# Optimization experiments

Hardware: AMD Instinct MI355X
Metric: run time of the kernel (lower is better)

Reference implementation:

```python
import jax, jax.numpy as jnp
import numpy as np

B_SZ, SEQ, H = 8, 1024, 2048
LN_EPS = 1e-6
CLIP = 1.0e6


def setup_inputs() -> dict:
    key = jax.random.key(0)
    ks = jax.random.split(key, 8)
    lecun = 1.0 / np.sqrt(H)
    return {
        "x": jax.random.normal(ks[0], (B_SZ, SEQ, H), dtype=jnp.float32),
        "context": jnp.zeros((B_SZ, H), dtype=jnp.float32),
        # learned params
        "A": -jax.random.uniform(ks[1], (H,), dtype=jnp.float32),  # diagonal decay (zeros-init in src; small negative for stable decay)
        "Bm": jax.random.normal(ks[2], (H, H), dtype=jnp.float32) * lecun,
        "Cm": jax.random.normal(ks[3], (H, H), dtype=jnp.float32) * lecun,
        "dt_kernel": jax.random.normal(ks[4], (H, 1), dtype=jnp.float32) * 0.02,
        "dt_bias": jnp.zeros((1,), dtype=jnp.float32),
        "gate_kernel": jax.random.normal(ks[5], (H, H), dtype=jnp.float32) * lecun,
        "gate_bias": jnp.zeros((H,), dtype=jnp.float32),
        "ln_scale": jnp.ones((H,), dtype=jnp.float32),
        "ln_bias": jnp.zeros((H,), dtype=jnp.float32),
    }


def _layernorm(x, scale, bias):
    mu = jnp.mean(x, axis=-1, keepdims=True)
    var = jnp.mean(jnp.square(x - mu), axis=-1, keepdims=True)
    return (x - mu) * jax.lax.rsqrt(var + LN_EPS) * scale + bias


def reference(x, context, A, Bm, Cm, dt_kernel, dt_bias, gate_kernel, gate_bias, ln_scale, ln_bias):
    xn = jnp.clip(_layernorm(x, ln_scale, ln_bias), -CLIP, CLIP)  # [B,S,H]
    xt = jnp.swapaxes(xn, 0, 1)  # time-major [S,B,H]

    def step(state, x_t):
        # x_t: [B,H]; delta: [B,1] from Dense(1)
        delta = jnp.exp(x_t @ dt_kernel + dt_bias)
        decay = jnp.exp(delta * A)                  # [B,H] via broadcast
        new_state = state * decay + x_t @ Bm        # [B,H]
        out = new_state @ Cm                        # [B,H]
        return new_state, out

    final_state, ys = jax.lax.scan(step, context, xt)
    outputs = jnp.swapaxes(ys, 0, 1)  # [B,S,H]
    gate = outputs @ gate_kernel + gate_bias
    outputs = outputs * jax.nn.sigmoid(gate)  # GLU
    # dropout deterministic (training=False) -> identity
    return outputs, final_state
```

## Files before the change

### kernel.cpp

```cpp
#include <hip/hip_runtime.h>
#include <hip/hip_bf16.h>

#define H_DIM 2048
#define B_SZ  8
#define SEQ   1024
#define M_DIM (B_SZ*SEQ)
#define KDIM  2048
#define NKT   (KDIM/64)
#define CCH   32
#define CLEN  (SEQ/CCH)

using f32x4 = __attribute__((ext_vector_type(4))) float;
using s16x8 = __attribute__((ext_vector_type(8))) short;

__device__ __forceinline__ float bf2f(unsigned short u) {
  unsigned int x = ((unsigned int)u) << 16;
  return __builtin_bit_cast(float, x);
}
__device__ __forceinline__ unsigned short f2bf(float f) {
  unsigned int x = __builtin_bit_cast(unsigned int, f);
  unsigned int r = (x + 0x7fffu + ((x >> 16) & 1u)) >> 16;
  return (unsigned short)r;
}

__device__ __forceinline__ void gl_lds16(const void* g, void* l) {
  __builtin_amdgcn_global_load_lds(
      (__attribute__((address_space(1))) void*)g,
      (__attribute__((address_space(3))) void*)l, 16, 0, 0);
}

__global__ __launch_bounds__(256) void transpose_kernel(
    const float* __restrict__ src, unsigned short* __restrict__ dst, int R, int C)
{
  __shared__ float t[32][33];
  int tx = threadIdx.x & 31, ty = threadIdx.x >> 5;
  int c0 = blockIdx.x << 5, r0 = blockIdx.y << 5;
#pragma unroll
  for (int i = 0; i < 32; i += 8)
    t[ty + i][tx] = src[(size_t)(r0 + ty + i) * C + (c0 + tx)];
  __syncthreads();
#pragma unroll
  for (int i = 0; i < 32; i += 8)
    dst[(size_t)(c0 + ty + i) * R + (r0 + tx)] = f2bf(t[tx][ty + i]);
}

__global__ __launch_bounds__(256) void ln_delta_kernel(
    const float* __restrict__ x, const float* __restrict__ lns,
    const float* __restrict__ lnb, const float* __restrict__ dtk,
    const float* __restrict__ dtb, unsigned short* __restrict__ xn,
    float* __restrict__ delta)
{
  const int row = blockIdx.x;
  const int tid = threadIdx.x;
  const float* xr = x + (size_t)row * H_DIM;
  float v[8];
  *(float4*)&v[0] = ((const float4*)xr)[tid * 2];
  *(float4*)&v[4] = ((const float4*)xr)[tid * 2 + 1];
  float s1 = 0.f, s2 = 0.f;
#pragma unroll
  for (int j = 0; j < 8; ++j) { s1 += v[j]; s2 += v[j] * v[j]; }
  __shared__ float red[8];
#pragma unroll
  for (int off = 32; off; off >>= 1) {
    s1 += __shfl_down(s1, off);
    s2 += __shfl_down(s2, off);
  }
  if ((tid & 63) == 0) { red[tid >> 6] = s1; red[4 + (tid >> 6)] = s2; }
  __syncthreads();
  float mean = (red[0] + red[1] + red[2] + red[3]) * (1.0f / H_DIM);
  float var  = (red[4] + red[5] + red[6] + red[7]) * (1.0f / H_DIM) - mean * mean;
  float rstd = rsqrtf(var + 1e-6f);

  float sc[8], bi[8], dk[8];
  *(float4*)&sc[0] = ((const float4*)lns)[tid * 2];
  *(float4*)&sc[4] = ((const float4*)lns)[tid * 2 + 1];
  *(float4*)&bi[0] = ((const float4*)lnb)[tid * 2];
  *(float4*)&bi[4] = ((const float4*)lnb)[tid * 2 + 1];
  *(float4*)&dk[0] = ((const float4*)dtk)[tid * 2];
  *(float4*)&dk[4] = ((const float4*)dtk)[tid * 2 + 1];

  float dot = 0.f;
  s16x8 o;
#pragma unroll
  for (int j = 0; j < 8; ++j) {
    float xv = (v[j] - mean) * rstd * sc[j] + bi[j];
    xv = fminf(fmaxf(xv, -1.0e6f), 1.0e6f);
    dot += xv * dk[j];
    o[j] = (short)f2bf(xv);
  }
  *(s16x8*)(xn + (size_t)row * H_DIM + tid * 8) = o;

  __syncthreads();
#pragma unroll
  for (int off = 32; off; off >>= 1) dot += __shfl_down(dot, off);
  if ((tid & 63) == 0) red[tid >> 6] = dot;
  __syncthreads();
  if (tid == 0)
    delta[row] = __expf(red[0] + red[1] + red[2] + red[3] + dtb[0]);
}

__global__ __launch_bounds__(256) void scan1_kernel(
    const unsigned short* __restrict__ U, const float* __restrict__ delta,
    const float* __restrict__ Adiag, float* __restrict__ Q, float* __restrict__ P)
{
  const int h = blockIdx.x * 1024 + threadIdx.x * 4;
  const int c = blockIdx.y, b = blockIdx.z;
  const float4 a = *(const float4*)(Adiag + h);
  const unsigned short* u = U + ((size_t)b * SEQ + c * CLEN) * H_DIM + h;
  const float* dl = delta + b * SEQ + c * CLEN;
  float4 st = {0.f, 0.f, 0.f, 0.f};
  float4 pr = {1.f, 1.f, 1.f, 1.f};
#pragma unroll 8
  for (int s = 0; s < CLEN; ++s) {
    const float d = dl[s];
    const ushort4 uv = *(const ushort4*)(u + (size_t)s * H_DIM);
    const float dx = __expf(d * a.x), dy = __expf(d * a.y);
    const float dz = __expf(d * a.z), dw = __expf(d * a.w);
    st.x = fmaf(st.x, dx, bf2f(uv.x)); st.y = fmaf(st.y, dy, bf2f(uv.y));
    st.z = fmaf(st.z, dz, bf2f(uv.z)); st.w = fmaf(st.w, dw, bf2f(uv.w));
    pr.x *= dx; pr.y *= dy; pr.z *= dz; pr.w *= dw;
  }
  const size_t idx = ((size_t)b * CCH + c) * H_DIM + h;
  *(float4*)(Q + idx) = st;
  *(float4*)(P + idx) = pr;
}

__global__ __launch_bounds__(256) void scan2_kernel(
    const float* __restrict__ Q, const float* __restrict__ P,
    const float* __restrict__ ctx, float* __restrict__ sIn,
    float* __restrict__ finalSt)
{
  const int h = blockIdx.x * 256 + threadIdx.x;
  const int b = blockIdx.y;
  float s = ctx[b * H_DIM + h];
#pragma unroll
  for (int c = 0; c < CCH; ++c) {
    const size_t idx = ((size_t)b * CCH + c) * H_DIM + h;
    sIn[idx] = s;
    s = fmaf(s, P[idx], Q[idx]);
  }
  finalSt[b * H_DIM + h] = s;
}

__global__ __launch_bounds__(256) void scan3_kernel(
    const unsigned short* __restrict__ U, const float* __restrict__ delta,
    const float* __restrict__ Adiag, const float* __restrict__ sIn,
    unsigned short* __restrict__ states)
{
  const int h = blockIdx.x * 1024 + threadIdx.x * 4;
  const int c = blockIdx.y, b = blockIdx.z;
  const float4 a = *(const float4*)(Adiag + h);
  const unsigned short* u = U + ((size_t)b * SEQ + c * CLEN) * H_DIM + h;
  unsigned short* so = states + ((size_t)b * SEQ + c * CLEN) * H_DIM + h;
  const float* dl = delta + b * SEQ + c * CLEN;
  float4 st = *(const float4*)(sIn + ((size_t)b * CCH + c) * H_DIM + h);
#pragma unroll 8
  for (int s = 0; s < CLEN; ++s) {
    const float d = dl[s];
    const ushort4 uv = *(const ushort4*)(u + (size_t)s * H_DIM);
    const float dx = __expf(d * a.x), dy = __expf(d * a.y);
    const float dz = __expf(d * a.z), dw = __expf(d * a.w);
    st.x = fmaf(st.x, dx, bf2f(uv.x)); st.y = fmaf(st.y, dy, bf2f(uv.y));
    st.z = fmaf(st.z, dz, bf2f(uv.z)); st.w = fmaf(st.w, dw, bf2f(uv.w));
    ushort4 ov = { f2bf(st.x), f2bf(st.y), f2bf(st.z), f2bf(st.w) };
    *(ushort4*)(so + (size_t)s * H_DIM) = ov;
  }
}


#define BARR()  __builtin_amdgcn_s_barrier();
#define LGKM0() asm volatile("s_waitcnt lgkmcnt(0)");
#define VMC(N)  asm volatile("s_waitcnt vmcnt(" #N ")" ::: "memory");

#define RD_A03(PA0, PA1) { _Pragma("unroll") for (int i_ = 0; i_ < 4; ++i_) { \
    a0[i_] = *(const s16x8*)((PA0) + i_ * 4096); \
    a1[i_] = *(const s16x8*)((PA1) + i_ * 4096); } }
#define RD_A47(PA0, PA1) { _Pragma("unroll") for (int i_ = 0; i_ < 4; ++i_) { \
    a0[i_] = *(const s16x8*)((PA0) + 16384 + i_ * 4096); \
    a1[i_] = *(const s16x8*)((PA1) + 16384 + i_ * 4096); } }
#define RD_B01(PB0, PB1) { _Pragma("unroll") for (int j_ = 0; j_ < 2; ++j_) { \
    bq0[j_] = *(const s16x8*)((PB0) + j_ * 8192); \
    bq1[j_] = *(const s16x8*)((PB1) + j_ * 8192); } }
#define RD_B23(PB0, PB1) { _Pragma("unroll") for (int j_ = 2; j_ < 4; ++j_) { \
    bq0[j_] = *(const s16x8*)((PB0) + j_ * 8192); \
    bq1[j_] = *(const s16x8*)((PB1) + j_ * 8192); } }

#define Q_MM(IB, JB) { __builtin_amdgcn_s_setprio(1); \
  _Pragma("unroll") for (int i_ = 0; i_ < 4; ++i_) \
  _Pragma("unroll") for (int j_ = 0; j_ < 2; ++j_) { \
    acc[(IB)+i_][(JB)+j_] = __builtin_amdgcn_mfma_f32_16x16x32_bf16(a0[i_], bq0[(JB)+j_], acc[(IB)+i_][(JB)+j_], 0, 0, 0); \
    acc[(IB)+i_][(JB)+j_] = __builtin_amdgcn_mfma_f32_16x16x32_bf16(a1[i_], bq1[(JB)+j_], acc[(IB)+i_][(JB)+j_], 0, 0, 0); } \
  __builtin_amdgcn_s_setprio(0); }

#define PH(QM) { BARR(); LGKM0(); QM; BARR(); }

#define STAGE_A(BUF, HH, TT) { const char* s_ = srcA + (HH) * 524288 + (TT) * 128; \
  char* d_ = ldsA + (BUF) * 32768 + (HH) * 16384 + tid16; \
  gl_lds16(s_, d_); gl_lds16(s_ + 262144, d_ + 8192); }
#define STAGE_B(BUF, HH, TT) { const char* s_ = srcB + (HH) * 524288 + (TT) * 128; \
  char* d_ = ldsB + (BUF) * 32768 + (HH) * 16384 + tid16; \
  gl_lds16(s_, d_); gl_lds16(s_ + 262144, d_ + 8192); }

template <int EPI>
__global__ __launch_bounds__(512, 2) void gemm8p(
    const char* __restrict__ Ab, const char* __restrict__ Bb,
    float* __restrict__ outF, unsigned short* __restrict__ outH,
    const unsigned short* __restrict__ Ybf, const float* __restrict__ gbias)
{
  extern __shared__ char lds[];
  char* ldsA = lds;
  char* ldsB = lds + 65536;

  const int tid  = threadIdx.x;
  const int lane = tid & 63, wid = tid >> 6;
  const int wr = wid >> 2, wc = wid & 3;
  const int fr = lane & 15, kq = lane >> 4;

  const int bid = blockIdx.x;
  const int xcd = bid & 7;
  const int li  = bid >> 3;
  const int bm  = (xcd >> 1) * 8 + (li & 7);
  const int bn  = (xcd & 1) * 4 + (li >> 3);

  const int grow = tid >> 3;
  const int gswz = ((tid & 7) ^ (grow & 7)) << 4;
  const char* srcA = Ab + ((size_t)(bm * 256 + grow)) * 4096 + gswz;
  const char* srcB = Bb + ((size_t)(bn * 256 + grow)) * 4096 + gswz;
  const int tid16 = tid << 4;

  const int sw0 = ((kq ^ (fr & 7)) << 4);
  const int sw1 = (((4 | kq) ^ (fr & 7)) << 4);
  const char* pa0b0 = ldsA + wr * 2048 + fr * 128 + sw0;
  const char* pa1b0 = ldsA + wr * 2048 + fr * 128 + sw1;
  const char* pa0b1 = pa0b0 + 32768;
  const char* pa1b1 = pa1b0 + 32768;
  const char* pb0b0 = ldsB + wc * 2048 + fr * 128 + sw0;
  const char* pb1b0 = ldsB + wc * 2048 + fr * 128 + sw1;
  const char* pb0b1 = pb0b0 + 32768;
  const char* pb1b1 = pb1b0 + 32768;

  f32x4 acc[8][4] = {};
  s16x8 a0[4], a1[4], bq0[4], bq1[4];

  STAGE_A(0, 0, 0); STAGE_B(0, 0, 0); STAGE_B(0, 1, 0); STAGE_A(0, 1, 0);
  STAGE_A(1, 0, 1); STAGE_B(1, 0, 1); STAGE_B(1, 1, 1);
  VMC(6);
  BARR();

  for (int t = 0; t < NKT / 2 - 1; ++t) {
    const int T0 = 2 * t;
    RD_A03(pa0b0, pa1b0); RD_B01(pb0b0, pb1b0);
    STAGE_A(1, 1, T0 + 1);
    PH(Q_MM(0, 0));
    RD_B23(pb0b0, pb1b0);
    STAGE_A(0, 0, T0 + 2);
    PH(Q_MM(0, 2));
    RD_A47(pa0b0, pa1b0);
    STAGE_B(0, 0, T0 + 2);
    PH(Q_MM(4, 0));
    STAGE_B(0, 1, T0 + 2);
    BARR(); Q_MM(4, 2); VMC(6); BARR();
    RD_A03(pa0b1, pa1b1); RD_B01(pb0b1, pb1b1);
    STAGE_A(0, 1, T0 + 2);
    PH(Q_MM(0, 0));
    RD_B23(pb0b1, pb1b1);
    STAGE_A(1, 0, T0 + 3);
    PH(Q_MM(0, 2));
    RD_A47(pa0b1, pa1b1);
    STAGE_B(1, 0, T0 + 3);
    PH(Q_MM(4, 0));
    STAGE_B(1, 1, T0 + 3);
    BARR(); Q_MM(4, 2); VMC(6); BARR();
  }

  RD_A03(pa0b0, pa1b0); RD_B01(pb0b0, pb1b0);
  STAGE_A(1, 1, 31);
  PH(Q_MM(0, 0));
  RD_B23(pb0b0, pb1b0);
  PH(Q_MM(0, 2));
  RD_A47(pa0b0, pa1b0);
  PH(Q_MM(4, 0));
  BARR(); Q_MM(4, 2); VMC(0); BARR();
  RD_A03(pa0b1, pa1b1); RD_B01(pb0b1, pb1b1);
  PH(Q_MM(0, 0));
  RD_B23(pb0b1, pb1b1);
  PH(Q_MM(0, 2));
  RD_A47(pa0b1, pa1b1);
  PH(Q_MM(4, 0));
  LGKM0();
  Q_MM(4, 2);

  __syncthreads();
  const int cr = (lane >> 4) << 2;
  const int cc = lane & 15;
  if constexpr (EPI == 1) {
#pragma unroll
    for (int i = 0; i < 8; ++i)
#pragma unroll
      for (int j = 0; j < 4; ++j)
#pragma unroll
        for (int r = 0; r < 4; ++r) {
          const int row = (2 * i + wr) * 16 + cr + r;
          const int col = (4 * j + wc) * 16 + cc;
          const int off = (row * 512 + col * 2) ^ ((row & 7) << 4);
          *(unsigned short*)(lds + off) = f2bf(acc[i][j][r]);
        }
    __syncthreads();
#pragma unroll
    for (int it = 0; it < 16; ++it) {
      const int L = it * 8192 + tid * 16;
      const int row = L >> 9, inrow = L & 511;
      const s16x8 v = *(const s16x8*)(lds + (L ^ ((row & 7) << 4)));
      *(s16x8*)(outH + ((size_t)(bm * 256 + row)) * H_DIM + bn * 256 + (inrow >> 1)) = v;
    }
  } else {
#pragma unroll
    for (int p = 0; p < 2; ++p) {
      if (p) __syncthreads();
#pragma unroll
      for (int i = 4 * p; i < 4 * p + 4; ++i)
#pragma unroll
        for (int j = 0; j < 4; ++j)
#pragma unroll
          for (int r = 0; r < 4; ++r) {
            const int lrow = (2 * i + wr) * 16 + cr + r - 128 * p;
            const int col = (4 * j + wc) * 16 + cc;
            const int off = (lrow * 1024 + col * 4) ^ ((lrow & 7) << 4);
            *(float*)(lds + off) = acc[i][j][r];
          }
      __syncthreads();
#pragma unroll
      for (int it = 0; it < 16; ++it) {
        const int L = it * 8192 + tid * 16;
        const int lrow = L >> 10, inrow = L & 1023;
        const f32x4 v = *(const f32x4*)(lds + (L ^ ((lrow & 7) << 4)));
        const size_t growg = (size_t)(bm * 256 + 128 * p + lrow);
        const int gcol = bn * 256 + (inrow >> 2);
        const float4 gb4 = *(const float4*)(gbias + gcol);
        const ushort4 y4 = *(const ushort4*)(Ybf + growg * H_DIM + gcol);
        float4 o;
        o.x = bf2f(y4.x) / (1.f + __expf(-(v[0] + gb4.x)));
        o.y = bf2f(y4.y) / (1.f + __expf(-(v[1] + gb4.y)));
        o.z = bf2f(y4.z) / (1.f + __expf(-(v[2] + gb4.z)));
        o.w = bf2f(y4.w) / (1.f + __expf(-(v[3] + gb4.w)));
        *(float4*)(outF + growg * H_DIM + gcol) = o;
      }
    }
  }
}

extern "C" void kernel_launch(void* const* d_in, const int* in_sizes, int n_in,
                              void* d_out, int out_size, void* d_ws, size_t ws_size,
                              hipStream_t stream) {
  (void)in_sizes; (void)n_in; (void)out_size; (void)ws_size;
  const float* x     = (const float*)d_in[0];
  const float* ctx   = (const float*)d_in[1];
  const float* Adiag = (const float*)d_in[2];
  const float* Bm    = (const float*)d_in[3];
  const float* Cm    = (const float*)d_in[4];
  const float* dtk   = (const float*)d_in[5];
  const float* dtb   = (const float*)d_in[6];
  const float* gk    = (const float*)d_in[7];
  const float* gb    = (const float*)d_in[8];
  const float* lns   = (const float*)d_in[9];
  const float* lnb   = (const float*)d_in[10];
  float* outF = (float*)d_out;

  char* ws = (char*)d_ws;
  unsigned short* xnY    = (unsigned short*)ws; ws += (size_t)M_DIM * H_DIM * 2;
  unsigned short* U      = (unsigned short*)ws; ws += (size_t)M_DIM * H_DIM * 2;
  unsigned short* states = (unsigned short*)ws; ws += (size_t)M_DIM * H_DIM * 2;
  unsigned short* T1     = (unsigned short*)ws; ws += (size_t)H_DIM * H_DIM * 2;
  unsigned short* T2     = (unsigned short*)ws; ws += (size_t)H_DIM * H_DIM * 2;
  unsigned short* T3     = (unsigned short*)ws; ws += (size_t)H_DIM * H_DIM * 2;
  float* delta           = (float*)ws;          ws += (size_t)M_DIM * 4;
  float* Qbuf            = (float*)ws;          ws += (size_t)B_SZ * CCH * H_DIM * 4;
  float* Pbuf            = (float*)ws;          ws += (size_t)B_SZ * CCH * H_DIM * 4;
  float* sInBuf          = (float*)ws;          ws += (size_t)B_SZ * CCH * H_DIM * 4;

  hipFuncSetAttribute((const void*)&gemm8p<1>,
                      hipFuncAttributeMaxDynamicSharedMemorySize, 131072);
  hipFuncSetAttribute((const void*)&gemm8p<2>,
                      hipFuncAttributeMaxDynamicSharedMemorySize, 131072);

  dim3 tb(256);
  transpose_kernel<<<dim3(64, 64), tb, 0, stream>>>(Bm, T1, H_DIM, H_DIM);
  transpose_kernel<<<dim3(64, 64), tb, 0, stream>>>(Cm, T2, H_DIM, H_DIM);
  transpose_kernel<<<dim3(64, 64), tb, 0, stream>>>(gk, T3, H_DIM, H_DIM);
  ln_delta_kernel<<<M_DIM, tb, 0, stream>>>(x, lns, lnb, dtk, dtb, xnY, delta);
  gemm8p<1><<<256, 512, 131072, stream>>>(
      (const char*)xnY, (const char*)T1, nullptr, U, nullptr, nullptr);
  scan1_kernel<<<dim3(H_DIM / 1024, CCH, B_SZ), tb, 0, stream>>>(
      U, delta, Adiag, Qbuf, Pbuf);
  scan2_kernel<<<dim3(H_DIM / 256, B_SZ), tb, 0, stream>>>(
      Qbuf, Pbuf, ctx, sInBuf, outF + (size_t)M_DIM * H_DIM);
  scan3_kernel<<<dim3(H_DIM / 1024, CCH, B_SZ), tb, 0, stream>>>(
      U, delta, Adiag, sInBuf, states);
  gemm8p<1><<<256, 512, 131072, stream>>>(
      (const char*)states, (const char*)T2, nullptr, xnY, nullptr, nullptr);
  gemm8p<2><<<256, 512, 131072, stream>>>(
      (const char*)xnY, (const char*)T3, outF, nullptr, xnY, gb);
}
```

Measured before the change: 257.3 us.

## Software-pipeline LDS fragment reads one phase ahead of MFMA in GEMM loop

Restructures the GEMM main loop so LDS fragment reads for the next MFMA phase are issued before the current phase's MFMAs, using separate register sets for the A and B fragments. The explicit lgkmcnt waits and the double barriers per phase are removed, leaving one vmcnt wait plus barrier per phase. The goal is to hide LDS read latency behind matrix math. In exchange it uses more fragment registers, which can raise register pressure at 2 waves per SIMD. LDS buffer reuse must stay correct under the looser barrier placement.

```diff
diff --git a/kernel.cpp b/kernel.cpp
--- a/kernel.cpp
+++ b/kernel.cpp
@@ -169,30 +169,21 @@
 
 
 #define BARR()  __builtin_amdgcn_s_barrier();
-#define LGKM0() asm volatile("s_waitcnt lgkmcnt(0)");
 #define VMC(N)  asm volatile("s_waitcnt vmcnt(" #N ")" ::: "memory");
 
-#define RD_A03(PA0, PA1) { _Pragma("unroll") for (int i_ = 0; i_ < 4; ++i_) { \
-    a0[i_] = *(const s16x8*)((PA0) + i_ * 4096); \
-    a1[i_] = *(const s16x8*)((PA1) + i_ * 4096); } }
-#define RD_A47(PA0, PA1) { _Pragma("unroll") for (int i_ = 0; i_ < 4; ++i_) { \
-    a0[i_] = *(const s16x8*)((PA0) + 16384 + i_ * 4096); \
-    a1[i_] = *(const s16x8*)((PA1) + 16384 + i_ * 4096); } }
-#define RD_B01(PB0, PB1) { _Pragma("unroll") for (int j_ = 0; j_ < 2; ++j_) { \
-    bq0[j_] = *(const s16x8*)((PB0) + j_ * 8192); \
-    bq1[j_] = *(const s16x8*)((PB1) + j_ * 8192); } }
-#define RD_B23(PB0, PB1) { _Pragma("unroll") for (int j_ = 2; j_ < 4; ++j_) { \
-    bq0[j_] = *(const s16x8*)((PB0) + j_ * 8192); \
-    bq1[j_] = *(const s16x8*)((PB1) + j_ * 8192); } }
-
-#define Q_MM(IB, JB) { __builtin_amdgcn_s_setprio(1); \
+#define RD_A(DST, PL, PHH, OFF) { _Pragma("unroll") for (int i_ = 0; i_ < 4; ++i_) { \
+    DST[0][i_] = *(const s16x8*)((PL) + (OFF) + i_ * 4096); \
+    DST[1][i_] = *(const s16x8*)((PHH) + (OFF) + i_ * 4096); } }
+#define RD_B(DST, PL, PHH, OFF) { _Pragma("unroll") for (int j_ = 0; j_ < 2; ++j_) { \
+    DST[0][j_] = *(const s16x8*)((PL) + (OFF) + j_ * 8192); \
+    DST[1][j_] = *(const s16x8*)((PHH) + (OFF) + j_ * 8192); } }
+
+#define QMM(IB, JB, AF, BF) { __builtin_amdgcn_s_setprio(1); \
   _Pragma("unroll") for (int i_ = 0; i_ < 4; ++i_) \
   _Pragma("unroll") for (int j_ = 0; j_ < 2; ++j_) { \
-    acc[(IB)+i_][(JB)+j_] = __builtin_amdgcn_mfma_f32_16x16x32_bf16(a0[i_], bq0[(JB)+j_], acc[(IB)+i_][(JB)+j_], 0, 0, 0); \
-    acc[(IB)+i_][(JB)+j_] = __builtin_amdgcn_mfma_f32_16x16x32_bf16(a1[i_], bq1[(JB)+j_], acc[(IB)+i_][(JB)+j_], 0, 0, 0); } \
+    acc[(IB)+i_][(JB)+j_] = __builtin_amdgcn_mfma_f32_16x16x32_bf16(AF[0][i_], BF[0][j_], acc[(IB)+i_][(JB)+j_], 0, 0, 0); \
+    acc[(IB)+i_][(JB)+j_] = __builtin_amdgcn_mfma_f32_16x16x32_bf16(AF[1][i_], BF[1][j_], acc[(IB)+i_][(JB)+j_], 0, 0, 0); } \
   __builtin_amdgcn_s_setprio(0); }
-
-#define PH(QM) { BARR(); LGKM0(); QM; BARR(); }
 
 #define STAGE_A(BUF, HH, TT) { const char* s_ = srcA + (HH) * 524288 + (TT) * 128; \
   char* d_ = ldsA + (BUF) * 32768 + (HH) * 16384 + tid16; \
@@ -240,55 +231,68 @@
   const char* pb1b1 = pb1b0 + 32768;
 
   f32x4 acc[8][4] = {};
-  s16x8 a0[4], a1[4], bq0[4], bq1[4];
+  s16x8 a03[2][4], a47[2][4], b01a[2][2], b01b[2][2], b23[2][2];
 
   STAGE_A(0, 0, 0); STAGE_B(0, 0, 0); STAGE_B(0, 1, 0); STAGE_A(0, 1, 0);
   STAGE_A(1, 0, 1); STAGE_B(1, 0, 1); STAGE_B(1, 1, 1);
   VMC(6);
   BARR();
+  RD_A(a03, pa0b0, pa1b0, 0);
+  RD_B(b01a, pb0b0, pb1b0, 0);
 
   for (int t = 0; t < NKT / 2 - 1; ++t) {
     const int T0 = 2 * t;
-    RD_A03(pa0b0, pa1b0); RD_B01(pb0b0, pb1b0);
+    RD_B(b23, pb0b0, pb1b0, 16384);
     STAGE_A(1, 1, T0 + 1);
-    PH(Q_MM(0, 0));
-    RD_B23(pb0b0, pb1b0);
+    QMM(0, 0, a03, b01a);
+    VMC(6); BARR();
+    RD_A(a47, pa0b0, pa1b0, 16384);
     STAGE_A(0, 0, T0 + 2);
-    PH(Q_MM(0, 2));
-    RD_A47(pa0b0, pa1b0);
+    QMM(0, 2, a03, b23);
+    VMC(6); BARR();
+    RD_B(b01b, pb0b1, pb1b1, 0);
     STAGE_B(0, 0, T0 + 2);
-    PH(Q_MM(4, 0));
+    QMM(4, 0, a47, b01a);
+    VMC(6); BARR();
+    RD_A(a03, pa0b1, pa1b1, 0);
     STAGE_B(0, 1, T0 + 2);
-    BARR(); Q_MM(4, 2); VMC(6); BARR();
-    RD_A03(pa0b1, pa1b1); RD_B01(pb0b1, pb1b1);
+    QMM(4, 2, a47, b23);
+    VMC(6); BARR();
+    RD_B(b23, pb0b1, pb1b1, 16384);
     STAGE_A(0, 1, T0 + 2);
-    PH(Q_MM(0, 0));
-    RD_B23(pb0b1, pb1b1);
+    QMM(0, 0, a03, b01b);
+    VMC(6); BARR();
+    RD_A(a47, pa0b1, pa1b1, 16384);
     STAGE_A(1, 0, T0 + 3);
-    PH(Q_MM(0, 2));
-    RD_A47(pa0b1, pa1b1);
+    QMM(0, 2, a03, b23);
+    VMC(6); BARR();
+    RD_B(b01a, pb0b0, pb1b0, 0);
     STAGE_B(1, 0, T0 + 3);
-    PH(Q_MM(4, 0));
+    QMM(4, 0, a47, b01b);
+    VMC(6); BARR();
+    RD_A(a03, pa0b0, pa1b0, 0);
     STAGE_B(1, 1, T0 + 3);
-    BARR(); Q_MM(4, 2); VMC(6); BARR();
-  }
-
-  RD_A03(pa0b0, pa1b0); RD_B01(pb0b0, pb1b0);
+    QMM(4, 2, a47, b23);
+    VMC(6); BARR();
+  }
+
+  RD_B(b23, pb0b0, pb1b0, 16384);
   STAGE_A(1, 1, 31);
-  PH(Q_MM(0, 0));
-  RD_B23(pb0b0, pb1b0);
-  PH(Q_MM(0, 2));
-  RD_A47(pa0b0, pa1b0);
-  PH(Q_MM(4, 0));
-  BARR(); Q_MM(4, 2); VMC(0); BARR();
-  RD_A03(pa0b1, pa1b1); RD_B01(pb0b1, pb1b1);
-  PH(Q_MM(0, 0));
-  RD_B23(pb0b1, pb1b1);
-  PH(Q_MM(0, 2));
-  RD_A47(pa0b1, pa1b1);
-  PH(Q_MM(4, 0));
-  LGKM0();
-  Q_MM(4, 2);
+  QMM(0, 0, a03, b01a);
+  VMC(6); BARR();
+  RD_A(a47, pa0b0, pa1b0, 16384);
+  QMM(0, 2, a03, b23);
+  VMC(0); BARR();
+  RD_B(b01b, pb0b1, pb1b1, 0);
+  QMM(4, 0, a47, b01a);
+  RD_A(a03, pa0b1, pa1b1, 0);
+  QMM(4, 2, a47, b23);
+  RD_B(b23, pb0b1, pb1b1, 16384);
+  QMM(0, 0, a03, b01b);
+  RD_A(a47, pa0b1, pa1b1, 16384);
+  QMM(0, 2, a03, b23);
+  QMM(4, 0, a47, b01b);
+  QMM(4, 2, a47, b23);
 
   __syncthreads();
   const int cr = (lane >> 4) << 2;
```

Measured after the change: 259.7 us. About the same (+0.9%).
